# Performance work log

Hardware: AMD Instinct MI355X
Metric: run time of the kernel (lower is better)

The kernel has to match this reference:

```python
import jax, jax.numpy as jnp
import numpy as np

B, T = 4, 2048          # batch, seq_len
D, H = 2048, 4096       # input_dim, router hidden_dim
E, O = 16, 2048         # num_experts, expert_output_dim
TAU = 0.5               # forward default tau


def setup_inputs() -> dict:
    key = jax.random.key(0)
    kx, k1, k2, k3, k4, k5, k6 = jax.random.split(key, 7)
    s = 0.02
    return {
        "x": jax.random.normal(kx, (B, T, D), dtype=jnp.float32),
        "W1": jax.random.normal(k1, (D, H), dtype=jnp.float32) * s,
        "b1": jnp.zeros((H,), dtype=jnp.float32),
        "W2": jax.random.normal(k2, (H, E), dtype=jnp.float32) * s,
        "b2": jnp.zeros((E,), dtype=jnp.float32),
        "We": jax.random.normal(k3, (E, D, O), dtype=jnp.float32) * s,
        "be": jnp.zeros((E, O), dtype=jnp.float32),
    }


def reference(x, W1, b1, W2, b2, We, be):
    # Router: Linear -> ReLU -> Linear -> softmax
    h = jax.nn.relu(jnp.einsum("btd,dh->bth", x, W1) + b1)
    logits = jnp.einsum("bth,he->bte", h, W2) + b2
    probs = jax.nn.softmax(logits, axis=-1)                 # [B,T,E]
    max_p = jnp.max(probs, axis=-1, keepdims=True)
    mask = probs >= TAU * max_p                              # [B,T,E] bool
    k_per_token = jnp.sum(mask, axis=-1)                     # [B,T] int
    gates = jnp.where(mask, probs, 0.0)                      # masked router probs
    # Per-expert dense Linear, masked weighted accumulate (E=16 is a fixed,
    # structurally distinct set; loop is over experts, not data dims).
    out = jnp.zeros((B, T, O), dtype=x.dtype)
    for i in range(E):
        expert_out = jnp.einsum("btd,do->bto", x, We[i]) + be[i]
        out = out + gates[..., i:i + 1] * expert_out
    return out, k_per_token
```

## Files before the change

kernel.cpp:

```cpp
#include <hip/hip_runtime.h>
#include <stdint.h>

#define M_TOK 8192
#define DDIM  2048
#define HDIM  4096
#define NEXP  16
#define ODIM  2048

typedef __attribute__((ext_vector_type(8))) __bf16 bf16x8;
typedef __attribute__((ext_vector_type(4))) float  f32x4;

__device__ __forceinline__ unsigned short f2bf(float f) {
    unsigned int u = __float_as_uint(f);
    unsigned int r = (u + 0x7FFFu + ((u >> 16) & 1u)) >> 16;
    return (unsigned short)r;
}
__device__ __forceinline__ float bf2f(unsigned short s) {
    return __uint_as_float(((unsigned int)s) << 16);
}

template <int CTRL>
__device__ __forceinline__ float dpp_add(float x) {
    int yi = __builtin_amdgcn_update_dpp(0, __float_as_int(x), CTRL, 0xF, 0xF, true);
    return x + __int_as_float(yi);
}


__global__ void split_x_kernel(const float* __restrict__ x,
                               ushort* __restrict__ xh, ushort* __restrict__ xl) {
    size_t i = ((size_t)blockIdx.x * 256 + threadIdx.x) * 4;
    float4 v = *(const float4*)(x + i);
    float f[4] = {v.x, v.y, v.z, v.w};
    ushort hu[4], lu[4];
#pragma unroll
    for (int u = 0; u < 4; ++u) {
        hu[u] = f2bf(f[u]);
        lu[u] = f2bf(f[u] - bf2f(hu[u]));
    }
    *(ushort4*)(xh + i) = make_ushort4(hu[0], hu[1], hu[2], hu[3]);
    *(ushort4*)(xl + i) = make_ushort4(lu[0], lu[1], lu[2], lu[3]);
}

__global__ void transpose_split_w1_kernel(const float* __restrict__ W1,
                                          ushort* __restrict__ th, ushort* __restrict__ tl) {
    __shared__ float tile[64][65];
    int h0 = (blockIdx.x & 63) * 64;
    int d0 = (blockIdx.x >> 6) * 64;
    int r = threadIdx.x >> 4;
    int c = (threadIdx.x & 15) * 4;
#pragma unroll
    for (int rr = 0; rr < 4; ++rr) {
        int row = rr * 16 + r;
        float4 v = *(const float4*)(W1 + (size_t)(d0 + row) * HDIM + h0 + c);
        tile[row][c + 0] = v.x; tile[row][c + 1] = v.y;
        tile[row][c + 2] = v.z; tile[row][c + 3] = v.w;
    }
    __syncthreads();
#pragma unroll
    for (int rr = 0; rr < 4; ++rr) {
        int hrow = rr * 16 + r;
        ushort hu[4], lu[4];
#pragma unroll
        for (int u = 0; u < 4; ++u) {
            float f = tile[c + u][hrow];
            hu[u] = f2bf(f);
            lu[u] = f2bf(f - bf2f(hu[u]));
        }
        size_t o = (size_t)(h0 + hrow) * DDIM + d0 + c;
        *(ushort4*)(th + o) = make_ushort4(hu[0], hu[1], hu[2], hu[3]);
        *(ushort4*)(tl + o) = make_ushort4(lu[0], lu[1], lu[2], lu[3]);
    }
}

__global__ void transpose_we_kernel(const float* __restrict__ We, ushort* __restrict__ wt) {
    __shared__ float tile[64][65];
    int e = blockIdx.y;
    int o0 = (blockIdx.x & 31) * 64;
    int d0 = (blockIdx.x >> 5) * 64;
    const float* src = We + (size_t)e * DDIM * ODIM;
    ushort* dst = wt + (size_t)e * ODIM * DDIM;
    int r = threadIdx.x >> 4;
    int c = (threadIdx.x & 15) * 4;
#pragma unroll
    for (int rr = 0; rr < 4; ++rr) {
        int row = rr * 16 + r;
        float4 v = *(const float4*)(src + (size_t)(d0 + row) * ODIM + o0 + c);
        tile[row][c + 0] = v.x; tile[row][c + 1] = v.y;
        tile[row][c + 2] = v.z; tile[row][c + 3] = v.w;
    }
    __syncthreads();
#pragma unroll
    for (int rr = 0; rr < 4; ++rr) {
        int orow = rr * 16 + r;
        ushort hu[4];
#pragma unroll
        for (int u = 0; u < 4; ++u) hu[u] = f2bf(tile[c + u][orow]);
        *(ushort4*)(dst + (size_t)(o0 + orow) * DDIM + d0 + c) =
            make_ushort4(hu[0], hu[1], hu[2], hu[3]);
    }
}


__device__ __forceinline__ void stage_tile(const ushort* __restrict__ g0, int ld,
                                           ushort* lds0, int wave, int lane) {
#pragma unroll
    for (int j = 0; j < 4; ++j) {
        int L = wave * 256 + j * 64 + lane;
        int m = L >> 3;
        int kc = (L & 7) ^ (m & 7);
        const ushort* gp = g0 + (size_t)m * ld + kc * 8;
        ushort* lp = lds0 + (size_t)(wave * 256 + j * 64) * 8;
        __builtin_amdgcn_global_load_lds(
            (const __attribute__((address_space(1))) void*)gp,
            (__attribute__((address_space(3))) void*)lp, 16, 0, 0);
    }
}

__device__ __forceinline__ bf16x8 ldfrag(const ushort* lds0, int row, int kc) {
    return *(const bf16x8*)(lds0 + ((row << 3) + (kc ^ (row & 7))) * 8);
}

__global__ __launch_bounds__(256, 2) void gemm1_kernel(
    const ushort* __restrict__ xh, const ushort* __restrict__ xl,
    const ushort* __restrict__ wh, const ushort* __restrict__ wl,
    const float* __restrict__ b1, const float* __restrict__ W2,
    float* __restrict__ logits) {
    __shared__ ushort As[8192];
    __shared__ ushort Bs[8192];
    const int tile_m = (blockIdx.x & 63) << 7;
    const int tile_n = (blockIdx.x >> 6) << 7;
    const int tid = threadIdx.x;
    const int wave = tid >> 6, lane = tid & 63;
    const int q = lane >> 4, mrow = lane & 15;
    const int wm = (wave >> 1) << 6, wn = (wave & 1) << 6;
    f32x4 acc[4][4];
#pragma unroll
    for (int i = 0; i < 4; ++i)
#pragma unroll
        for (int j = 0; j < 4; ++j) acc[i][j] = {0.f, 0.f, 0.f, 0.f};

    for (int it = 0; it < 96; ++it) {
        const int phase = it >> 5;
        const ushort* Ab = (phase == 1) ? xl : xh;
        const ushort* Bb = (phase == 2) ? wl : wh;
        const int k0 = (it & 31) << 6;
        __syncthreads();
        stage_tile(Ab + (size_t)tile_m * DDIM + k0, DDIM, As, wave, lane);
        stage_tile(Bb + (size_t)tile_n * DDIM + k0, DDIM, Bs, wave, lane);
        __syncthreads();
#pragma unroll
        for (int s = 0; s < 2; ++s) {
            bf16x8 af[4], bfr[4];
#pragma unroll
            for (int i = 0; i < 4; ++i) af[i] = ldfrag(As, wm + i * 16 + mrow, s * 4 + q);
#pragma unroll
            for (int j = 0; j < 4; ++j) bfr[j] = ldfrag(Bs, wn + j * 16 + mrow, s * 4 + q);
#pragma unroll
            for (int i = 0; i < 4; ++i)
#pragma unroll
                for (int j = 0; j < 4; ++j)
                    acc[i][j] = __builtin_amdgcn_mfma_f32_16x16x32_bf16(
                        af[i], bfr[j], acc[i][j], 0, 0, 0);
        }
    }

    float b1v[4];
    f32x4 w2r[4][4];
#pragma unroll
    for (int j = 0; j < 4; ++j) {
        const int cc = tile_n + wn + j * 16 + mrow;
        b1v[j] = b1[cc];
        const float4* wp = (const float4*)(W2 + (size_t)cc * NEXP);
#pragma unroll
        for (int qq = 0; qq < 4; ++qq) {
            float4 v = wp[qq];
            w2r[j][qq] = (f32x4){v.x, v.y, v.z, v.w};
        }
    }
    __syncthreads();
    float* part = (float*)As;
    const int w01 = wave & 1;
#pragma unroll
    for (int i = 0; i < 4; ++i) {
#pragma unroll
        for (int r = 0; r < 4; ++r) {
            const int rl = wm + i * 16 + q * 4 + r;
            float ll[16];
#pragma unroll
            for (int e = 0; e < 16; ++e) ll[e] = 0.f;
#pragma unroll
            for (int j = 0; j < 4; ++j) {
                float v = acc[i][j][r] + b1v[j];
                v = v > 0.f ? v : 0.f;
#pragma unroll
                for (int e = 0; e < 16; ++e)
                    ll[e] = fmaf(v, w2r[j][e >> 2][e & 3], ll[e]);
            }
#pragma unroll
            for (int e = 0; e < 16; ++e) {
                float v = ll[e];
                v = dpp_add<0xB1>(v);
                v = dpp_add<0x4E>(v);
                v = dpp_add<0x124>(v);
                v = dpp_add<0x128>(v);
                ll[e] = v;
            }
            if (mrow == 0) {
                float4* dst = (float4*)(part + ((size_t)(w01 * 128 + rl)) * 16);
                dst[0] = make_float4(ll[0],  ll[1],  ll[2],  ll[3]);
                dst[1] = make_float4(ll[4],  ll[5],  ll[6],  ll[7]);
                dst[2] = make_float4(ll[8],  ll[9],  ll[10], ll[11]);
                dst[3] = make_float4(ll[12], ll[13], ll[14], ll[15]);
            }
        }
    }
    __syncthreads();
    for (int idx = tid; idx < 2048; idx += 256) {
        float s = part[idx] + part[2048 + idx];
        atomicAdd(&logits[(size_t)(tile_m + (idx >> 4)) * NEXP + (idx & 15)], s);
    }
}

__global__ void gates_kernel(const float* __restrict__ logits,
                             const float* __restrict__ b2,
                             float* __restrict__ gates, float* __restrict__ kout,
                             int* __restrict__ cnt, int* __restrict__ list) {
    const int t = blockIdx.x * 256 + threadIdx.x;
    float l[16];
    const float4* lp = (const float4*)(logits + (size_t)t * 16);
#pragma unroll
    for (int i = 0; i < 4; ++i) {
        float4 v = lp[i];
        l[i * 4] = v.x; l[i * 4 + 1] = v.y; l[i * 4 + 2] = v.z; l[i * 4 + 3] = v.w;
    }
#pragma unroll
    for (int i = 0; i < 16; ++i) l[i] += b2[i];
    float lmax = l[0];
#pragma unroll
    for (int i = 1; i < 16; ++i) lmax = fmaxf(lmax, l[i]);
    float p[16], S = 0.f;
#pragma unroll
    for (int i = 0; i < 16; ++i) { p[i] = expf(l[i] - lmax); S += p[i]; }
#pragma unroll
    for (int i = 0; i < 16; ++i) p[i] /= S;
    float pmax = p[0];
#pragma unroll
    for (int i = 1; i < 16; ++i) pmax = fmaxf(pmax, p[i]);
    const float thr = 0.5f * pmax;
    int k = 0;
    float g[16];
#pragma unroll
    for (int i = 0; i < 16; ++i) {
        bool m = p[i] >= thr;
        g[i] = m ? p[i] : 0.f;
        k += m ? 1 : 0;
        if (m) {
            int pos = atomicAdd(&cnt[i], 1);
            list[i * M_TOK + pos] = t;
        }
    }
    float4* gp = (float4*)(gates + (size_t)t * 16);
#pragma unroll
    for (int i = 0; i < 4; ++i)
        gp[i] = make_float4(g[i * 4], g[i * 4 + 1], g[i * 4 + 2], g[i * 4 + 3]);
    kout[t] = (float)k;
}

__global__ void init_out_kernel(const float* __restrict__ gates,
                                const float* __restrict__ be, float* __restrict__ out) {
    const int t = blockIdx.x;
    const int tid = threadIdx.x;
    __shared__ float g[16];
    if (tid < 16) g[tid] = gates[(size_t)t * 16 + tid];
    __syncthreads();
    const int c0 = tid * 8;
    float a[8] = {0.f, 0.f, 0.f, 0.f, 0.f, 0.f, 0.f, 0.f};
#pragma unroll
    for (int e = 0; e < 16; ++e) {
        float ge = g[e];
        if (ge != 0.f) {
            float4 v1 = *(const float4*)(be + (size_t)e * ODIM + c0);
            float4 v2 = *(const float4*)(be + (size_t)e * ODIM + c0 + 4);
            a[0] = fmaf(ge, v1.x, a[0]); a[1] = fmaf(ge, v1.y, a[1]);
            a[2] = fmaf(ge, v1.z, a[2]); a[3] = fmaf(ge, v1.w, a[3]);
            a[4] = fmaf(ge, v2.x, a[4]); a[5] = fmaf(ge, v2.y, a[5]);
            a[6] = fmaf(ge, v2.z, a[6]); a[7] = fmaf(ge, v2.w, a[7]);
        }
    }
    *(float4*)(out + (size_t)t * ODIM + c0)     = make_float4(a[0], a[1], a[2], a[3]);
    *(float4*)(out + (size_t)t * ODIM + c0 + 4) = make_float4(a[4], a[5], a[6], a[7]);
}

__global__ __launch_bounds__(256, 3) void moe_sparse_kernel(
    const ushort* __restrict__ xh, const ushort* __restrict__ weT,
    const float* __restrict__ gates, const int* __restrict__ cnt,
    const int* __restrict__ list, float* __restrict__ out) {
    const int bx = blockIdx.x;
    const int e = bx >> 10;
    const int chunk = (bx >> 4) & 63;
    const int ntile = bx & 15;
    const int ce = cnt[e];
    const int row0 = chunk << 7;
    if (row0 >= ce) return;
    const int rows = min(128, ce - row0);

    __shared__ ushort As[8192];
    __shared__ ushort Bs[8192];
    __shared__ int toks[128];
    __shared__ float gv[128];

    const int tid = threadIdx.x;
    if (tid < 128) {
        int t = list[e * M_TOK + row0 + min(tid, rows - 1)];
        toks[tid] = t;
        gv[tid] = gates[(size_t)t * NEXP + e];
    }
    __syncthreads();

    const int wave = tid >> 6, lane = tid & 63;
    const int q = lane >> 4, mrow = lane & 15;
    const int wm = (wave >> 1) << 6, wn = (wave & 1) << 6;

    const ushort* agp[4];
    const ushort* bgp[4];
    ushort* alp[4];
    ushort* blp[4];
    const ushort* wbase = weT + ((size_t)e * ODIM + (ntile << 7)) * DDIM;
#pragma unroll
    for (int j = 0; j < 4; ++j) {
        int L = wave * 256 + j * 64 + lane;
        int m = L >> 3;
        int kc = (L & 7) ^ (m & 7);
        agp[j] = xh + (size_t)toks[m] * DDIM + kc * 8;
        bgp[j] = wbase + (size_t)m * DDIM + kc * 8;
        alp[j] = As + (size_t)L * 8;
        blp[j] = Bs + (size_t)L * 8;
    }

    f32x4 acc[4][4];
#pragma unroll
    for (int i = 0; i < 4; ++i)
#pragma unroll
        for (int j = 0; j < 4; ++j) acc[i][j] = {0.f, 0.f, 0.f, 0.f};

    for (int it = 0; it < 32; ++it) {
        const int k0 = it << 6;
        __syncthreads();
#pragma unroll
        for (int j = 0; j < 4; ++j) {
            __builtin_amdgcn_global_load_lds(
                (const __attribute__((address_space(1))) void*)(agp[j] + k0),
                (__attribute__((address_space(3))) void*)alp[j], 16, 0, 0);
            __builtin_amdgcn_global_load_lds(
                (const __attribute__((address_space(1))) void*)(bgp[j] + k0),
                (__attribute__((address_space(3))) void*)blp[j], 16, 0, 0);
        }
        __syncthreads();
#pragma unroll
        for (int s = 0; s < 2; ++s) {
            bf16x8 af[4], bfr[4];
#pragma unroll
            for (int i = 0; i < 4; ++i) af[i] = ldfrag(As, wm + i * 16 + mrow, s * 4 + q);
#pragma unroll
            for (int j = 0; j < 4; ++j) bfr[j] = ldfrag(Bs, wn + j * 16 + mrow, s * 4 + q);
#pragma unroll
            for (int i = 0; i < 4; ++i)
#pragma unroll
                for (int j = 0; j < 4; ++j)
                    acc[i][j] = __builtin_amdgcn_mfma_f32_16x16x32_bf16(
                        af[i], bfr[j], acc[i][j], 0, 0, 0);
        }
    }

#pragma unroll
    for (int i = 0; i < 4; ++i) {
        const int rl = wm + i * 16 + q * 4;
#pragma unroll
        for (int r = 0; r < 4; ++r) {
            const int lrow = rl + r;
            if (lrow < rows) {
                const int t = toks[lrow];
                const float g = gv[lrow];
                float* orow = out + (size_t)t * ODIM + (ntile << 7) + wn + mrow;
#pragma unroll
                for (int j = 0; j < 4; ++j)
                    atomicAdd(orow + j * 16, g * acc[i][j][r]);
            }
        }
    }
}

extern "C" void kernel_launch(void* const* d_in, const int* in_sizes, int n_in,
                              void* d_out, int out_size, void* d_ws, size_t ws_size,
                              hipStream_t stream) {
    const float* x  = (const float*)d_in[0];
    const float* W1 = (const float*)d_in[1];
    const float* b1 = (const float*)d_in[2];
    const float* W2 = (const float*)d_in[3];
    const float* b2 = (const float*)d_in[4];
    const float* We = (const float*)d_in[5];
    const float* be = (const float*)d_in[6];
    float* out  = (float*)d_out;
    float* kout = out + (size_t)M_TOK * ODIM;

    char* ws = (char*)d_ws;
    ushort* x_hi   = (ushort*)(ws);
    ushort* x_lo   = (ushort*)(ws + 33554432);
    ushort* w1t_hi = (ushort*)(ws + 67108864);
    ushort* w1t_lo = (ushort*)(ws + 83886080);
    int*    cnt    = (int*)   (ws + 83886080);
    int*    list   = (int*)   (ws + 83887104);
    ushort* weT    = (ushort*)(ws + 100663296);
    float*  logits = (float*) (ws + 234881024);
    float*  gates  = (float*) (ws + 235405312);

    hipMemsetAsync(logits, 0, (size_t)M_TOK * NEXP * sizeof(float), stream);
    split_x_kernel<<<16384, 256, 0, stream>>>(x, x_hi, x_lo);
    transpose_split_w1_kernel<<<2048, 256, 0, stream>>>(W1, w1t_hi, w1t_lo);
    gemm1_kernel<<<2048, 256, 0, stream>>>(x_hi, x_lo, w1t_hi, w1t_lo, b1, W2, logits);
    hipMemsetAsync(cnt, 0, 64, stream);
    gates_kernel<<<32, 256, 0, stream>>>(logits, b2, gates, kout, cnt, list);
    dim3 gwe(1024, 16);
    transpose_we_kernel<<<gwe, 256, 0, stream>>>(We, weT);
    init_out_kernel<<<M_TOK, 256, 0, stream>>>(gates, be, out);
    moe_sparse_kernel<<<16384, 256, 0, stream>>>(x_hi, weT, gates, cnt, list, out);
}
```

Before: 1.208 ms.

## Double-buffer gemm1 LDS tiles and use a transpose-style reduction for router logits

```diff
diff --git a/kernel.cpp b/kernel.cpp
--- a/kernel.cpp
+++ b/kernel.cpp
@@ -20,9 +20,12 @@
 }
 
 template <int CTRL>
-__device__ __forceinline__ float dpp_add(float x) {
-    int yi = __builtin_amdgcn_update_dpp(0, __float_as_int(x), CTRL, 0xF, 0xF, true);
-    return x + __int_as_float(yi);
+__device__ __forceinline__ float dpp_mov(float x) {
+    return __int_as_float(
+        __builtin_amdgcn_update_dpp(0, __float_as_int(x), CTRL, 0xF, 0xF, true));
+}
+__device__ __forceinline__ float swz_xor4(float x) {
+    return __int_as_float(__builtin_amdgcn_ds_swizzle(__float_as_int(x), 0x101F));
 }
 
 
@@ -120,13 +123,34 @@
     return *(const bf16x8*)(lds0 + ((row << 3) + (kc ^ (row & 7))) * 8);
 }
 
+__device__ __forceinline__ void mfma_step(const ushort* As, const ushort* Bs,
+                                          int wm, int wn, int mrow, int q,
+                                          f32x4 (&acc)[4][4]) {
+#pragma unroll
+    for (int s = 0; s < 2; ++s) {
+        bf16x8 af[4], bfr[4];
+#pragma unroll
+        for (int i = 0; i < 4; ++i) af[i] = ldfrag(As, wm + i * 16 + mrow, s * 4 + q);
+#pragma unroll
+        for (int j = 0; j < 4; ++j) bfr[j] = ldfrag(Bs, wn + j * 16 + mrow, s * 4 + q);
+#pragma unroll
+        for (int i = 0; i < 4; ++i)
+#pragma unroll
+            for (int j = 0; j < 4; ++j)
+                acc[i][j] = __builtin_amdgcn_mfma_f32_16x16x32_bf16(
+                    af[i], bfr[j], acc[i][j], 0, 0, 0);
+    }
+}
+
 __global__ __launch_bounds__(256, 2) void gemm1_kernel(
     const ushort* __restrict__ xh, const ushort* __restrict__ xl,
     const ushort* __restrict__ wh, const ushort* __restrict__ wl,
     const float* __restrict__ b1, const float* __restrict__ W2,
     float* __restrict__ logits) {
-    __shared__ ushort As[8192];
-    __shared__ ushort Bs[8192];
+    __shared__ ushort As0[8192];
+    __shared__ ushort Bs0[8192];
+    __shared__ ushort As1[8192];
+    __shared__ ushort Bs1[8192];
     const int tile_m = (blockIdx.x & 63) << 7;
     const int tile_n = (blockIdx.x >> 6) << 7;
     const int tid = threadIdx.x;
@@ -139,30 +163,27 @@
 #pragma unroll
         for (int j = 0; j < 4; ++j) acc[i][j] = {0.f, 0.f, 0.f, 0.f};
 
-    for (int it = 0; it < 96; ++it) {
-        const int phase = it >> 5;
-        const ushort* Ab = (phase == 1) ? xl : xh;
-        const ushort* Bb = (phase == 2) ? wl : wh;
-        const int k0 = (it & 31) << 6;
+#define SRC_A(t) ((((t) >> 5) == 1 ? xl : xh) + (size_t)tile_m * DDIM + (((t) & 31) << 6))
+#define SRC_B(t) ((((t) >> 5) == 2 ? wl : wh) + (size_t)tile_n * DDIM + (((t) & 31) << 6))
+
+    stage_tile(SRC_A(0), DDIM, As0, wave, lane);
+    stage_tile(SRC_B(0), DDIM, Bs0, wave, lane);
+    __syncthreads();
+
+    for (int it = 0; it < 96; it += 2) {
+        stage_tile(SRC_A(it + 1), DDIM, As1, wave, lane);
+        stage_tile(SRC_B(it + 1), DDIM, Bs1, wave, lane);
+        mfma_step(As0, Bs0, wm, wn, mrow, q, acc);
         __syncthreads();
-        stage_tile(Ab + (size_t)tile_m * DDIM + k0, DDIM, As, wave, lane);
-        stage_tile(Bb + (size_t)tile_n * DDIM + k0, DDIM, Bs, wave, lane);
+        if (it + 2 < 96) {
+            stage_tile(SRC_A(it + 2), DDIM, As0, wave, lane);
+            stage_tile(SRC_B(it + 2), DDIM, Bs0, wave, lane);
+        }
+        mfma_step(As1, Bs1, wm, wn, mrow, q, acc);
         __syncthreads();
-#pragma unroll
-        for (int s = 0; s < 2; ++s) {
-            bf16x8 af[4], bfr[4];
-#pragma unroll
-            for (int i = 0; i < 4; ++i) af[i] = ldfrag(As, wm + i * 16 + mrow, s * 4 + q);
-#pragma unroll
-            for (int j = 0; j < 4; ++j) bfr[j] = ldfrag(Bs, wn + j * 16 + mrow, s * 4 + q);
-#pragma unroll
-            for (int i = 0; i < 4; ++i)
-#pragma unroll
-                for (int j = 0; j < 4; ++j)
-                    acc[i][j] = __builtin_amdgcn_mfma_f32_16x16x32_bf16(
-                        af[i], bfr[j], acc[i][j], 0, 0, 0);
-        }
-    }
+    }
+#undef SRC_A
+#undef SRC_B
 
     float b1v[4];
     f32x4 w2r[4][4];
@@ -177,9 +198,11 @@
             w2r[j][qq] = (f32x4){v.x, v.y, v.z, v.w};
         }
     }
-    __syncthreads();
-    float* part = (float*)As;
+    float* part = (float*)As0;
     const int w01 = wave & 1;
+    const bool pb0 = (mrow & 1) != 0, pb1 = (mrow & 2) != 0;
+    const bool pb2 = (mrow & 4) != 0, pb3 = (mrow & 8) != 0;
+    const int E = (mrow & 3) | ((mrow & 8) >> 1) | ((mrow & 4) << 1);
 #pragma unroll
     for (int i = 0; i < 4; ++i) {
 #pragma unroll
@@ -196,21 +219,32 @@
                 for (int e = 0; e < 16; ++e)
                     ll[e] = fmaf(v, w2r[j][e >> 2][e & 3], ll[e]);
             }
-#pragma unroll
-            for (int e = 0; e < 16; ++e) {
-                float v = ll[e];
-                v = dpp_add<0xB1>(v);
-                v = dpp_add<0x4E>(v);
-                v = dpp_add<0x124>(v);
-                v = dpp_add<0x128>(v);
-                ll[e] = v;
-            }
-            if (mrow == 0) {
-                float4* dst = (float4*)(part + ((size_t)(w01 * 128 + rl)) * 16);
-                dst[0] = make_float4(ll[0],  ll[1],  ll[2],  ll[3]);
-                dst[1] = make_float4(ll[4],  ll[5],  ll[6],  ll[7]);
-                dst[2] = make_float4(ll[8],  ll[9],  ll[10], ll[11]);
-                dst[3] = make_float4(ll[12], ll[13], ll[14], ll[15]);
+            float s1[8];
+#pragma unroll
+            for (int e2 = 0; e2 < 8; ++e2) {
+                float a = ll[2 * e2], b = ll[2 * e2 + 1];
+                float y = pb0 ? b : a, z = pb0 ? a : b;
+                s1[e2] = y + dpp_mov<0xB1>(z);
+            }
+            float s2[4];
+#pragma unroll
+            for (int e2 = 0; e2 < 4; ++e2) {
+                float a = s1[2 * e2], b = s1[2 * e2 + 1];
+                float y = pb1 ? b : a, z = pb1 ? a : b;
+                s2[e2] = y + dpp_mov<0x4E>(z);
+            }
+            float s3[2];
+#pragma unroll
+            for (int e2 = 0; e2 < 2; ++e2) {
+                float a = s2[2 * e2], b = s2[2 * e2 + 1];
+                float y = pb3 ? b : a, z = pb3 ? a : b;
+                s3[e2] = y + dpp_mov<0x128>(z);
+            }
+            {
+                float a = s3[0], b = s3[1];
+                float y = pb2 ? b : a, z = pb2 ? a : b;
+                float fin = y + swz_xor4(z);
+                part[(size_t)(w01 * 128 + rl) * 16 + E] = fin;
             }
         }
     }
@@ -356,20 +390,7 @@
                 (__attribute__((address_space(3))) void*)blp[j], 16, 0, 0);
         }
         __syncthreads();
-#pragma unroll
-        for (int s = 0; s < 2; ++s) {
-            bf16x8 af[4], bfr[4];
-#pragma unroll
-            for (int i = 0; i < 4; ++i) af[i] = ldfrag(As, wm + i * 16 + mrow, s * 4 + q);
-#pragma unroll
-            for (int j = 0; j < 4; ++j) bfr[j] = ldfrag(Bs, wn + j * 16 + mrow, s * 4 + q);
-#pragma unroll
-            for (int i = 0; i < 4; ++i)
-#pragma unroll
-                for (int j = 0; j < 4; ++j)
-                    acc[i][j] = __builtin_amdgcn_mfma_f32_16x16x32_bf16(
-                        af[i], bfr[j], acc[i][j], 0, 0, 0);
-        }
+        mfma_step(As, Bs, wm, wn, mrow, q, acc);
     }
 
 #pragma unroll
```

After: 1.228 ms. About the same (+1.7%).
